# Optimization experiments

Hardware: AMD Instinct MI355X
Metric: run time of the kernel (lower is better)

The kernel has to match this reference:

```python
import jax, jax.numpy as jnp
import numpy as np

BLOCK = 128          # block_size in the source
FP8_MAX = 448.0      # max representable magnitude of float8_e4m3fn


def _quant_weight(w):
    """Pre-quantize a [N, K] float weight into fp8 values + per 128x128 block scales."""
    N, K = w.shape
    wb = w.reshape(N // BLOCK, BLOCK, K // BLOCK, BLOCK)
    w_scale = jnp.max(jnp.abs(wb), axis=(1, 3)) / FP8_MAX           # [Nb, Kb]
    s = jnp.where(w_scale == 0, 1.0, w_scale)
    wq = (wb / s[:, None, :, None]).astype(jnp.float8_e4m3fn).astype(jnp.float32)
    return wq.reshape(N, K), w_scale


def setup_inputs() -> dict:
    key = jax.random.key(0)
    kx, kw = jax.random.split(key)
    M, K, N = 16384, 2048, 2048
    x = jax.random.normal(kx, (M, K), dtype=jnp.float32)
    w = jax.random.normal(kw, (N, K), dtype=jnp.float32) * 0.02
    w_fp8, w_scale = _quant_weight(w)
    return {"x": x, "w_fp8": w_fp8, "w_scale": w_scale}


def reference(x, w_fp8, w_scale):
    """fp8 block-quantized linear: act_quant(x) then dequantized GEMM.

    x:       [M, K] float32 activations
    w_fp8:   [N, K] fp8-valued weight (stored as float32, exactly e4m3 representable)
    w_scale: [N/128, K/128] per-block weight scales
    """
    M, K = x.shape
    N = w_fp8.shape[0]
    # --- act_quant: per 128-element block along K, scale = amax / 448 ---
    xb = x.reshape(M, K // BLOCK, BLOCK)
    x_scale = jnp.max(jnp.abs(xb), axis=-1) / FP8_MAX               # [M, Kb]
    sx = jnp.where(x_scale == 0, 1.0, x_scale)
    xq = (xb / sx[..., None]).astype(jnp.float8_e4m3fn).astype(jnp.float32)
    # --- fp8_gemm with inline dequant: scales factor out per (m-block, n-block, k-block)
    # sum_kb sx[m,kb]*sw[nb,kb]*(xq . wq) == (xq*sx) @ (wq*sw)^T exactly ---
    x_deq = (xq * sx[..., None]).reshape(M, K)
    w_deq = (w_fp8.reshape(N // BLOCK, BLOCK, K // BLOCK, BLOCK)
             * w_scale[:, None, :, None]).reshape(N, K)
    return x_deq @ w_deq.T                                          # [M, N]
```

## Files before the change

kernel.cpp:

```cpp
#include <hip/hip_runtime.h>

#define M_DIM 16384
#define N_DIM 2048
#define K_DIM 2048
#define KB    (K_DIM / 128)

#define BM 256
#define BN 256
#define BK 64
#define NT (K_DIM / BK)

#define XGRID (M_DIM * K_DIM / 2048)
#define WGRID (N_DIM * K_DIM / 2048)

typedef __bf16 bf16x8 __attribute__((ext_vector_type(8)));
typedef float  f32x4  __attribute__((ext_vector_type(4)));
typedef int    i32x4  __attribute__((ext_vector_type(4)));

__device__ __forceinline__ unsigned short f32_to_bf16_rne(float f) {
    unsigned int u = __float_as_uint(f);
    u += 0x7FFFu + ((u >> 16) & 1u);
    return (unsigned short)(u >> 16);
}

__global__ __launch_bounds__(256) void quant_all_kernel(const float* __restrict__ x,
                                                        unsigned short* __restrict__ xdq,
                                                        const float* __restrict__ w,
                                                        const float* __restrict__ wscale,
                                                        unsigned short* __restrict__ wdq) {
    const int tid = threadIdx.x;
    if (blockIdx.x < XGRID) {
        const size_t base = ((size_t)blockIdx.x * 256 + tid) * 8;
        const float4 va = *(const float4*)(x + base);
        const float4 vb = *(const float4*)(x + base + 4);
        float amax = fmaxf(
            fmaxf(fmaxf(fabsf(va.x), fabsf(va.y)), fmaxf(fabsf(va.z), fabsf(va.w))),
            fmaxf(fmaxf(fabsf(vb.x), fabsf(vb.y)), fmaxf(fabsf(vb.z), fabsf(vb.w))));
#pragma unroll
        for (int m = 8; m >= 1; m >>= 1)
            amax = fmaxf(amax, __shfl_xor(amax, m, 64));
        float s = amax / 448.0f;
        if (s == 0.0f) s = 1.0f;
        const int p01 = __builtin_amdgcn_cvt_pk_fp8_f32(va.x / s, va.y / s, 0, false);
        const int p23 = __builtin_amdgcn_cvt_pk_fp8_f32(va.z / s, va.w / s, 0, false);
        const int p45 = __builtin_amdgcn_cvt_pk_fp8_f32(vb.x / s, vb.y / s, 0, false);
        const int p67 = __builtin_amdgcn_cvt_pk_fp8_f32(vb.z / s, vb.w / s, 0, false);
        uint4 out;
        out.x = (unsigned int)f32_to_bf16_rne(__builtin_amdgcn_cvt_f32_fp8(p01, 0) * s)
              | ((unsigned int)f32_to_bf16_rne(__builtin_amdgcn_cvt_f32_fp8(p01, 1) * s) << 16);
        out.y = (unsigned int)f32_to_bf16_rne(__builtin_amdgcn_cvt_f32_fp8(p23, 0) * s)
              | ((unsigned int)f32_to_bf16_rne(__builtin_amdgcn_cvt_f32_fp8(p23, 1) * s) << 16);
        out.z = (unsigned int)f32_to_bf16_rne(__builtin_amdgcn_cvt_f32_fp8(p45, 0) * s)
              | ((unsigned int)f32_to_bf16_rne(__builtin_amdgcn_cvt_f32_fp8(p45, 1) * s) << 16);
        out.w = (unsigned int)f32_to_bf16_rne(__builtin_amdgcn_cvt_f32_fp8(p67, 0) * s)
              | ((unsigned int)f32_to_bf16_rne(__builtin_amdgcn_cvt_f32_fp8(p67, 1) * s) << 16);
        *(uint4*)(xdq + base) = out;
    } else {
        const size_t e = ((size_t)(blockIdx.x - XGRID) * 256 + tid) * 8;
        const float4 va = *(const float4*)(w + e);
        const float4 vb = *(const float4*)(w + e + 4);
        const int n = (int)(e >> 11);
        const int k = (int)(e & 2047);
        const float s = wscale[(n >> 7) * KB + (k >> 7)];
        uint4 out;
        out.x = (unsigned int)f32_to_bf16_rne(va.x * s) | ((unsigned int)f32_to_bf16_rne(va.y * s) << 16);
        out.y = (unsigned int)f32_to_bf16_rne(va.z * s) | ((unsigned int)f32_to_bf16_rne(va.w * s) << 16);
        out.z = (unsigned int)f32_to_bf16_rne(vb.x * s) | ((unsigned int)f32_to_bf16_rne(vb.y * s) << 16);
        out.w = (unsigned int)f32_to_bf16_rne(vb.z * s) | ((unsigned int)f32_to_bf16_rne(vb.w * s) << 16);
        *(uint4*)(wdq + e) = out;
    }
}

__global__ __launch_bounds__(512, 2) void gemm_bt_kernel(const unsigned short* __restrict__ A,
                                                         const unsigned short* __restrict__ B,
                                                         float* __restrict__ C) {
    __shared__ __align__(16) unsigned short As[2][2][256][32];
    __shared__ __align__(16) unsigned short Bs[2][2][256][32];

    const int tid  = threadIdx.x;
    const int lane = tid & 63;
    const int wave = tid >> 6;
    const int wm   = (wave >> 2) * 128;
    const int wn   = (wave & 3) * 64;
    const int quad = lane >> 4;
    const int l16  = lane & 15;
    const int pc   = quad ^ ((l16 >> 1) & 3);

    const int m0 = blockIdx.x * BM;
    const int n0 = blockIdx.y * BN;

    f32x4 acc[8][4] = {};

    const int srow = tid >> 2;
    const int sc   = (tid & 3) ^ ((tid >> 3) & 3);
    const unsigned short* gA = A + (size_t)(m0 + srow) * K_DIM + sc * 8;
    const unsigned short* gB = B + (size_t)(n0 + srow) * K_DIM + sc * 8;

#define GLD(SRC, DST) __builtin_amdgcn_global_load_lds( \
    (__attribute__((address_space(1))) void*)(SRC), \
    (__attribute__((address_space(3))) void*)(DST), 16, 0, 0)

#define STG_A(DB, KH, KT) do { \
    GLD(gA + (size_t)(KT) * 64 + (KH) * 32,                       &As[DB][KH][wave * 16][0]); \
    GLD(gA + (size_t)128 * K_DIM + (size_t)(KT) * 64 + (KH) * 32, &As[DB][KH][128 + wave * 16][0]); \
  } while (0)
#define STG_B(DB, KH, KT) do { \
    GLD(gB + (size_t)(KT) * 64 + (KH) * 32,                       &Bs[DB][KH][wave * 16][0]); \
    GLD(gB + (size_t)128 * K_DIM + (size_t)(KT) * 64 + (KH) * 32, &Bs[DB][KH][128 + wave * 16][0]); \
  } while (0)

#define VMCNT(n) asm volatile("s_waitcnt vmcnt(" #n ")" ::: "memory")
#define BAR() __builtin_amdgcn_s_barrier()
#define LGKM(n) do { \
    asm volatile("s_waitcnt lgkmcnt(" #n ")" ::: "memory"); \
    __builtin_amdgcn_sched_barrier(0); \
  } while (0)

    i32x4 ae0, ae1, ae2, ae3, be0, be1, be2, be3;
    i32x4 ao0, ao1, ao2, ao3, bo0, bo1, bo2, bo3;
    i32x4 ax0, ax1, ax2, ax3;

    const unsigned aA = (unsigned)(unsigned long long)
        (__attribute__((address_space(3))) const void*)&As[0][0][wm + l16][pc * 8];
    const unsigned aB = (unsigned)(unsigned long long)
        (__attribute__((address_space(3))) const void*)&Bs[0][0][wn + l16][pc * 8];

#define DSR(D, BASE, IMM) \
    asm volatile("ds_read_b128 %0, %1 offset:%c2" : "=v"(D) : "v"(BASE), "i"(IMM))

#define RD_AX(BUF, KH) do { \
    DSR(ax0, aA, (BUF) * 32768 + (KH) * 16384 + 4096); \
    DSR(ax1, aA, (BUF) * 32768 + (KH) * 16384 + 5120); \
    DSR(ax2, aA, (BUF) * 32768 + (KH) * 16384 + 6144); \
    DSR(ax3, aA, (BUF) * 32768 + (KH) * 16384 + 7168); \
  } while (0)
#define RD_E(BUF, KH) do { \
    DSR(ae0, aA, (BUF) * 32768 + (KH) * 16384 + 0);    \
    DSR(ae1, aA, (BUF) * 32768 + (KH) * 16384 + 1024); \
    DSR(ae2, aA, (BUF) * 32768 + (KH) * 16384 + 2048); \
    DSR(ae3, aA, (BUF) * 32768 + (KH) * 16384 + 3072); \
    DSR(be0, aB, (BUF) * 32768 + (KH) * 16384 + 0);    \
    DSR(be1, aB, (BUF) * 32768 + (KH) * 16384 + 1024); \
    DSR(be2, aB, (BUF) * 32768 + (KH) * 16384 + 2048); \
    DSR(be3, aB, (BUF) * 32768 + (KH) * 16384 + 3072); \
  } while (0)
#define RD_O(BUF, KH) do { \
    DSR(ao0, aA, (BUF) * 32768 + (KH) * 16384 + 0);    \
    DSR(ao1, aA, (BUF) * 32768 + (KH) * 16384 + 1024); \
    DSR(ao2, aA, (BUF) * 32768 + (KH) * 16384 + 2048); \
    DSR(ao3, aA, (BUF) * 32768 + (KH) * 16384 + 3072); \
    DSR(bo0, aB, (BUF) * 32768 + (KH) * 16384 + 0);    \
    DSR(bo1, aB, (BUF) * 32768 + (KH) * 16384 + 1024); \
    DSR(bo2, aB, (BUF) * 32768 + (KH) * 16384 + 2048); \
    DSR(bo3, aB, (BUF) * 32768 + (KH) * 16384 + 3072); \
  } while (0)

#define BC(X) __builtin_bit_cast(bf16x8, X)
#define MMROW(I, AF, B0, B1, B2, B3) do { \
    acc[I][0] = __builtin_amdgcn_mfma_f32_16x16x32_bf16(BC(AF), BC(B0), acc[I][0], 0, 0, 0); \
    acc[I][1] = __builtin_amdgcn_mfma_f32_16x16x32_bf16(BC(AF), BC(B1), acc[I][1], 0, 0, 0); \
    acc[I][2] = __builtin_amdgcn_mfma_f32_16x16x32_bf16(BC(AF), BC(B2), acc[I][2], 0, 0, 0); \
    acc[I][3] = __builtin_amdgcn_mfma_f32_16x16x32_bf16(BC(AF), BC(B3), acc[I][3], 0, 0, 0); \
  } while (0)
#define MM16(I0, A0, A1, A2, A3, B0, B1, B2, B3) do { \
    __builtin_amdgcn_s_setprio(1); \
    MMROW((I0) + 0, A0, B0, B1, B2, B3); \
    MMROW((I0) + 1, A1, B0, B1, B2, B3); \
    MMROW((I0) + 2, A2, B0, B1, B2, B3); \
    MMROW((I0) + 3, A3, B0, B1, B2, B3); \
    __builtin_amdgcn_s_setprio(0); \
  } while (0)

#define TILE_STD(B_, KT1, KT2) do { \
    RD_AX(B_, 0);      STG_A((B_) ^ 1, 1, KT1); LGKM(4); MM16(0, ae0, ae1, ae2, ae3, be0, be1, be2, be3); VMCNT(6); BAR(); \
    RD_O(B_, 1);       STG_B((B_) ^ 1, 1, KT1); LGKM(8); MM16(4, ax0, ax1, ax2, ax3, be0, be1, be2, be3); BAR(); \
    RD_AX(B_, 1);      STG_A(B_, 0, KT2);       LGKM(4); MM16(0, ao0, ao1, ao2, ao3, bo0, bo1, bo2, bo3); VMCNT(6); BAR(); \
    RD_E((B_) ^ 1, 0); STG_B(B_, 0, KT2);       LGKM(8); MM16(4, ax0, ax1, ax2, ax3, bo0, bo1, bo2, bo3); BAR(); \
  } while (0)

    STG_A(0, 0, 0); STG_B(0, 0, 0);
    STG_A(0, 1, 0); STG_B(0, 1, 0);
    STG_A(1, 0, 1); STG_B(1, 0, 1);
    VMCNT(8);
    BAR();
    RD_E(0, 0);

#pragma unroll 1
    for (int t = 0; t < NT - 2; t += 2) {
        TILE_STD(0, t + 1, t + 2);
        TILE_STD(1, t + 2, t + 3);
    }
    RD_AX(0, 0); STG_A(1, 1, NT - 1); LGKM(4); MM16(0, ae0, ae1, ae2, ae3, be0, be1, be2, be3); VMCNT(6); BAR();
    RD_O(0, 1);  STG_B(1, 1, NT - 1); LGKM(8); MM16(4, ax0, ax1, ax2, ax3, be0, be1, be2, be3); BAR();
    RD_AX(0, 1);                      LGKM(4); MM16(0, ao0, ao1, ao2, ao3, bo0, bo1, bo2, bo3); VMCNT(4); BAR();
    RD_E(1, 0);                       LGKM(8); MM16(4, ax0, ax1, ax2, ax3, bo0, bo1, bo2, bo3); BAR();
    RD_AX(1, 0);                      LGKM(4); MM16(0, ae0, ae1, ae2, ae3, be0, be1, be2, be3); VMCNT(0); BAR();
    RD_O(1, 1);                       LGKM(8); MM16(4, ax0, ax1, ax2, ax3, be0, be1, be2, be3); BAR();
    RD_AX(1, 1);                      LGKM(4); MM16(0, ao0, ao1, ao2, ao3, bo0, bo1, bo2, bo3); BAR();
                                      LGKM(0); MM16(4, ax0, ax1, ax2, ax3, bo0, bo1, bo2, bo3);

#pragma unroll
    for (int i = 0; i < 8; ++i) {
        const int row = m0 + wm + i * 16 + quad * 4;
#pragma unroll
        for (int j = 0; j < 4; ++j) {
            const int col = n0 + wn + j * 16 + l16;
            float* cp = C + (size_t)row * N_DIM + col;
#pragma unroll
            for (int r = 0; r < 4; ++r)
                cp[(size_t)r * N_DIM] = acc[i][j][r];
        }
    }
}

extern "C" void kernel_launch(void* const* d_in, const int* in_sizes, int n_in,
                              void* d_out, int out_size, void* d_ws, size_t ws_size,
                              hipStream_t stream) {
    const float* x      = (const float*)d_in[0];
    const float* wfp8   = (const float*)d_in[1];
    const float* wscale = (const float*)d_in[2];
    float* out = (float*)d_out;

    unsigned short* xdq = (unsigned short*)d_ws;
    unsigned short* wdq = xdq + (size_t)M_DIM * K_DIM;

    quant_all_kernel<<<XGRID + WGRID, 256, 0, stream>>>(x, xdq, wfp8, wscale, wdq);
    gemm_bt_kernel<<<dim3(M_DIM / BM, N_DIM / BN), 512, 0, stream>>>(xdq, wdq, out);
}
```

Measured before the change: 349.9 us.

## Pre-swizzle weights into MFMA fragment layout and load B directly to registers

The weight dequant pass now writes bf16 weights in a fragment-tiled layout that matches the MFMA B-operand register order. The GEMM drops the B shared-memory buffers and loads B fragments straight from global memory into registers with global_load_dwordx4, prefetched one half-tile ahead. This halves LDS usage and removes the B LDS reads. In exchange, each wave redundantly fetches B from global/L2 and must wait on global latency in the inner loop.

```diff
diff --git a/kernel.cpp b/kernel.cpp
--- a/kernel.cpp
+++ b/kernel.cpp
@@ -67,7 +67,11 @@
         out.y = (unsigned int)f32_to_bf16_rne(va.z * s) | ((unsigned int)f32_to_bf16_rne(va.w * s) << 16);
         out.z = (unsigned int)f32_to_bf16_rne(vb.x * s) | ((unsigned int)f32_to_bf16_rne(vb.y * s) << 16);
         out.w = (unsigned int)f32_to_bf16_rne(vb.z * s) | ((unsigned int)f32_to_bf16_rne(vb.w * s) << 16);
-        *(uint4*)(wdq + e) = out;
+        const unsigned idx =
+            (((((unsigned)(n >> 6) * 32u + (unsigned)(k >> 6)) * 8u
+               + (unsigned)((n >> 4) & 3) * 2u + (unsigned)((k >> 5) & 1)) * 512u)
+             + (unsigned)((k >> 3) & 3) * 128u + (unsigned)(n & 15) * 8u);
+        *(uint4*)(wdq + idx) = out;
     }
 }
 
@@ -75,7 +79,6 @@
                                                          const unsigned short* __restrict__ B,
                                                          float* __restrict__ C) {
     __shared__ __align__(16) unsigned short As[2][2][256][32];
-    __shared__ __align__(16) unsigned short Bs[2][2][256][32];
 
     const int tid  = threadIdx.x;
     const int lane = tid & 63;
@@ -94,7 +97,9 @@
     const int srow = tid >> 2;
     const int sc   = (tid & 3) ^ ((tid >> 3) & 3);
     const unsigned short* gA = A + (size_t)(m0 + srow) * K_DIM + sc * 8;
-    const unsigned short* gB = B + (size_t)(n0 + srow) * K_DIM + sc * 8;
+
+    const unsigned short* p01 = B + ((size_t)(blockIdx.y * 4 + (wave & 3)) * 32) * 4096 + lane * 8;
+    const unsigned short* p23 = p01 + 2048;
 
 #define GLD(SRC, DST) __builtin_amdgcn_global_load_lds( \
     (__attribute__((address_space(1))) void*)(SRC), \
@@ -104,56 +109,47 @@
     GLD(gA + (size_t)(KT) * 64 + (KH) * 32,                       &As[DB][KH][wave * 16][0]); \
     GLD(gA + (size_t)128 * K_DIM + (size_t)(KT) * 64 + (KH) * 32, &As[DB][KH][128 + wave * 16][0]); \
   } while (0)
-#define STG_B(DB, KH, KT) do { \
-    GLD(gB + (size_t)(KT) * 64 + (KH) * 32,                       &Bs[DB][KH][wave * 16][0]); \
-    GLD(gB + (size_t)128 * K_DIM + (size_t)(KT) * 64 + (KH) * 32, &Bs[DB][KH][128 + wave * 16][0]); \
-  } while (0)
-
-#define VMCNT(n) asm volatile("s_waitcnt vmcnt(" #n ")" ::: "memory")
+
 #define BAR() __builtin_amdgcn_s_barrier()
-#define LGKM(n) do { \
-    asm volatile("s_waitcnt lgkmcnt(" #n ")" ::: "memory"); \
+#define WAIT2(VN, LN) do { \
+    asm volatile("s_waitcnt vmcnt(" #VN ") lgkmcnt(" #LN ")" ::: "memory"); \
     __builtin_amdgcn_sched_barrier(0); \
   } while (0)
-
-    i32x4 ae0, ae1, ae2, ae3, be0, be1, be2, be3;
-    i32x4 ao0, ao1, ao2, ao3, bo0, bo1, bo2, bo3;
+#define WAITL(LN) do { \
+    asm volatile("s_waitcnt lgkmcnt(" #LN ")" ::: "memory"); \
+    __builtin_amdgcn_sched_barrier(0); \
+  } while (0)
+#define WAITV(VN) do { \
+    asm volatile("s_waitcnt vmcnt(" #VN ")" ::: "memory"); \
+    __builtin_amdgcn_sched_barrier(0); \
+  } while (0)
+
+    i32x4 ae0, ae1, ae2, ae3;
+    i32x4 ao0, ao1, ao2, ao3;
     i32x4 ax0, ax1, ax2, ax3;
+    i32x4 be0, be1, be2, be3;
+    i32x4 bo0, bo1, bo2, bo3;
 
     const unsigned aA = (unsigned)(unsigned long long)
         (__attribute__((address_space(3))) const void*)&As[0][0][wm + l16][pc * 8];
-    const unsigned aB = (unsigned)(unsigned long long)
-        (__attribute__((address_space(3))) const void*)&Bs[0][0][wn + l16][pc * 8];
-
-#define DSR(D, BASE, IMM) \
-    asm volatile("ds_read_b128 %0, %1 offset:%c2" : "=v"(D) : "v"(BASE), "i"(IMM))
-
+
+#define DSR(D, IMM) \
+    asm volatile("ds_read_b128 %0, %1 offset:%c2" : "=v"(D) : "v"(aA), "i"(IMM))
+#define RD_AE(BUF) do { \
+    DSR(ae0, (BUF) * 32768 + 0);    DSR(ae1, (BUF) * 32768 + 1024); \
+    DSR(ae2, (BUF) * 32768 + 2048); DSR(ae3, (BUF) * 32768 + 3072); \
+  } while (0)
+#define RD_AO(BUF) do { \
+    DSR(ao0, (BUF) * 32768 + 16384 + 0);    DSR(ao1, (BUF) * 32768 + 16384 + 1024); \
+    DSR(ao2, (BUF) * 32768 + 16384 + 2048); DSR(ao3, (BUF) * 32768 + 16384 + 3072); \
+  } while (0)
 #define RD_AX(BUF, KH) do { \
-    DSR(ax0, aA, (BUF) * 32768 + (KH) * 16384 + 4096); \
-    DSR(ax1, aA, (BUF) * 32768 + (KH) * 16384 + 5120); \
-    DSR(ax2, aA, (BUF) * 32768 + (KH) * 16384 + 6144); \
-    DSR(ax3, aA, (BUF) * 32768 + (KH) * 16384 + 7168); \
-  } while (0)
-#define RD_E(BUF, KH) do { \
-    DSR(ae0, aA, (BUF) * 32768 + (KH) * 16384 + 0);    \
-    DSR(ae1, aA, (BUF) * 32768 + (KH) * 16384 + 1024); \
-    DSR(ae2, aA, (BUF) * 32768 + (KH) * 16384 + 2048); \
-    DSR(ae3, aA, (BUF) * 32768 + (KH) * 16384 + 3072); \
-    DSR(be0, aB, (BUF) * 32768 + (KH) * 16384 + 0);    \
-    DSR(be1, aB, (BUF) * 32768 + (KH) * 16384 + 1024); \
-    DSR(be2, aB, (BUF) * 32768 + (KH) * 16384 + 2048); \
-    DSR(be3, aB, (BUF) * 32768 + (KH) * 16384 + 3072); \
-  } while (0)
-#define RD_O(BUF, KH) do { \
-    DSR(ao0, aA, (BUF) * 32768 + (KH) * 16384 + 0);    \
-    DSR(ao1, aA, (BUF) * 32768 + (KH) * 16384 + 1024); \
-    DSR(ao2, aA, (BUF) * 32768 + (KH) * 16384 + 2048); \
-    DSR(ao3, aA, (BUF) * 32768 + (KH) * 16384 + 3072); \
-    DSR(bo0, aB, (BUF) * 32768 + (KH) * 16384 + 0);    \
-    DSR(bo1, aB, (BUF) * 32768 + (KH) * 16384 + 1024); \
-    DSR(bo2, aB, (BUF) * 32768 + (KH) * 16384 + 2048); \
-    DSR(bo3, aB, (BUF) * 32768 + (KH) * 16384 + 3072); \
-  } while (0)
+    DSR(ax0, (BUF) * 32768 + (KH) * 16384 + 4096); DSR(ax1, (BUF) * 32768 + (KH) * 16384 + 5120); \
+    DSR(ax2, (BUF) * 32768 + (KH) * 16384 + 6144); DSR(ax3, (BUF) * 32768 + (KH) * 16384 + 7168); \
+  } while (0)
+
+#define BLD(D, P, OFF) \
+    asm volatile("global_load_dwordx4 %0, %1, off offset:%c2" : "=v"(D) : "v"(P), "i"(OFF))
 
 #define BC(X) __builtin_bit_cast(bf16x8, X)
 #define MMROW(I, AF, B0, B1, B2, B3) do { \
@@ -172,32 +168,47 @@
   } while (0)
 
 #define TILE_STD(B_, KT1, KT2) do { \
-    RD_AX(B_, 0);      STG_A((B_) ^ 1, 1, KT1); LGKM(4); MM16(0, ae0, ae1, ae2, ae3, be0, be1, be2, be3); VMCNT(6); BAR(); \
-    RD_O(B_, 1);       STG_B((B_) ^ 1, 1, KT1); LGKM(8); MM16(4, ax0, ax1, ax2, ax3, be0, be1, be2, be3); BAR(); \
-    RD_AX(B_, 1);      STG_A(B_, 0, KT2);       LGKM(4); MM16(0, ao0, ao1, ao2, ao3, bo0, bo1, bo2, bo3); VMCNT(6); BAR(); \
-    RD_E((B_) ^ 1, 0); STG_B(B_, 0, KT2);       LGKM(8); MM16(4, ax0, ax1, ax2, ax3, bo0, bo1, bo2, bo3); BAR(); \
-  } while (0)
-
-    STG_A(0, 0, 0); STG_B(0, 0, 0);
-    STG_A(0, 1, 0); STG_B(0, 1, 0);
-    STG_A(1, 0, 1); STG_B(1, 0, 1);
-    VMCNT(8);
+    RD_AX(B_, 0); STG_A((B_) ^ 1, 1, KT1); BLD(bo0, p01, 1024); BLD(bo1, p01, 3072); \
+    WAIT2(4, 4); MM16(0, ae0, ae1, ae2, ae3, be0, be1, be2, be3); \
+    RD_AO(B_); BLD(bo2, p23, 1024); BLD(bo3, p23, 3072); \
+    WAITL(4); MM16(4, ax0, ax1, ax2, ax3, be0, be1, be2, be3); BAR(); \
+    p01 += 4096; p23 += 4096; \
+    RD_AX(B_, 1); STG_A(B_, 0, KT2); BLD(be0, p01, 0); BLD(be1, p01, 2048); \
+    WAIT2(4, 4); MM16(0, ao0, ao1, ao2, ao3, bo0, bo1, bo2, bo3); \
+    RD_AE((B_) ^ 1); BLD(be2, p23, 0); BLD(be3, p23, 2048); \
+    WAITL(4); MM16(4, ax0, ax1, ax2, ax3, bo0, bo1, bo2, bo3); BAR(); \
+  } while (0)
+
+    STG_A(0, 0, 0);
+    STG_A(0, 1, 0);
+    STG_A(1, 0, 1);
+    BLD(be0, p01, 0); BLD(be1, p01, 2048);
+    BLD(be2, p23, 0); BLD(be3, p23, 2048);
+    WAITV(0);
     BAR();
-    RD_E(0, 0);
+    RD_AE(0);
 
 #pragma unroll 1
     for (int t = 0; t < NT - 2; t += 2) {
         TILE_STD(0, t + 1, t + 2);
         TILE_STD(1, t + 2, t + 3);
     }
-    RD_AX(0, 0); STG_A(1, 1, NT - 1); LGKM(4); MM16(0, ae0, ae1, ae2, ae3, be0, be1, be2, be3); VMCNT(6); BAR();
-    RD_O(0, 1);  STG_B(1, 1, NT - 1); LGKM(8); MM16(4, ax0, ax1, ax2, ax3, be0, be1, be2, be3); BAR();
-    RD_AX(0, 1);                      LGKM(4); MM16(0, ao0, ao1, ao2, ao3, bo0, bo1, bo2, bo3); VMCNT(4); BAR();
-    RD_E(1, 0);                       LGKM(8); MM16(4, ax0, ax1, ax2, ax3, bo0, bo1, bo2, bo3); BAR();
-    RD_AX(1, 0);                      LGKM(4); MM16(0, ae0, ae1, ae2, ae3, be0, be1, be2, be3); VMCNT(0); BAR();
-    RD_O(1, 1);                       LGKM(8); MM16(4, ax0, ax1, ax2, ax3, be0, be1, be2, be3); BAR();
-    RD_AX(1, 1);                      LGKM(4); MM16(0, ao0, ao1, ao2, ao3, bo0, bo1, bo2, bo3); BAR();
-                                      LGKM(0); MM16(4, ax0, ax1, ax2, ax3, bo0, bo1, bo2, bo3);
+    RD_AX(0, 0); STG_A(1, 1, NT - 1); BLD(bo0, p01, 1024); BLD(bo1, p01, 3072);
+    WAIT2(4, 4); MM16(0, ae0, ae1, ae2, ae3, be0, be1, be2, be3);
+    RD_AO(0); BLD(bo2, p23, 1024); BLD(bo3, p23, 3072);
+    WAITL(4); MM16(4, ax0, ax1, ax2, ax3, be0, be1, be2, be3); BAR();
+    p01 += 4096; p23 += 4096;
+    RD_AX(0, 1); BLD(be0, p01, 0); BLD(be1, p01, 2048);
+    WAIT2(2, 4); MM16(0, ao0, ao1, ao2, ao3, bo0, bo1, bo2, bo3);
+    RD_AE(1); BLD(be2, p23, 0); BLD(be3, p23, 2048);
+    WAITL(4); MM16(4, ax0, ax1, ax2, ax3, bo0, bo1, bo2, bo3); BAR();
+    RD_AX(1, 0); BLD(bo0, p01, 1024); BLD(bo1, p01, 3072);
+    WAIT2(2, 4); MM16(0, ae0, ae1, ae2, ae3, be0, be1, be2, be3);
+    RD_AO(1); BLD(bo2, p23, 1024); BLD(bo3, p23, 3072);
+    WAITL(4); MM16(4, ax0, ax1, ax2, ax3, be0, be1, be2, be3); BAR();
+    RD_AX(1, 1);
+    WAIT2(0, 4); MM16(0, ao0, ao1, ao2, ao3, bo0, bo1, bo2, bo3);
+    WAITL(0); MM16(4, ax0, ax1, ax2, ax3, bo0, bo1, bo2, bo3);
 
 #pragma unroll
     for (int i = 0; i < 8; ++i) {
```

Result: slower. 357.5 us (+2.2%).
